# Performance work log

Hardware: AMD Instinct MI355X
Metric: run time of the kernel (lower is better)

## Reference

```python
import jax, jax.numpy as jnp
import numpy as np

N, E, C, K = 50000, 800000, 64, 8
D = C * K  # 512
NEG_SLOPE = 0.01  # torch leaky_relu default


def setup_inputs() -> dict:
    key = jax.random.key(0)
    ks = jax.random.split(key, 6)
    x = jax.random.normal(ks[0], (N, D), dtype=jnp.float32)
    edge_index = jax.random.randint(ks[1], (2, E), 0, N, dtype=jnp.int64)
    conv_W = jax.random.normal(ks[2], (K, C, C), dtype=jnp.float32) * (1.0 / np.sqrt(C))
    conv_b = jax.random.normal(ks[3], (K, C), dtype=jnp.float32) * 0.01
    W1 = jax.random.normal(ks[4], (D, D), dtype=jnp.float32) * (1.0 / np.sqrt(D))
    W2 = jax.random.normal(ks[5], (D, D), dtype=jnp.float32) * (1.0 / np.sqrt(D))
    return {"x": x, "edge_index": edge_index, "conv_W": conv_W,
            "conv_b": conv_b, "W1": W1, "W2": W2}


def _gcn_conv(xk, Wk, bk, src, dst, dinv, n):
    # PyG GCNConv: transform, then symmetric-normalized aggregation with self-loops,
    # then add bias.
    xt = xk @ Wk.T  # [N, C]
    norm = dinv[src] * dinv[dst]  # [E]
    agg = jax.ops.segment_sum(norm[:, None] * xt[src], dst, num_segments=n)
    agg = agg + (dinv * dinv)[:, None] * xt  # self-loop contribution
    return agg + bk


def reference(x, edge_index, conv_W, conv_b, W1, W2):
    n = x.shape[0]
    src, dst = edge_index[0], edge_index[1]
    # degree with self-loops (edge weight 1)
    deg = jax.ops.segment_sum(jnp.ones((E,), x.dtype), dst, num_segments=n) + 1.0
    dinv = deg ** -0.5
    xr = x.reshape(n, C, K)
    zs = [jax.nn.leaky_relu(_gcn_conv(xr[:, :, i], conv_W[i], conv_b[i], src, dst, dinv, n),
                            negative_slope=NEG_SLOPE)
          for i in range(K)]
    z = jnp.concatenate(zs, axis=1)  # [N, D]
    z = jax.nn.leaky_relu(z, negative_slope=NEG_SLOPE)
    # dropout is identity in eval mode (dr=12 is invalid for torch Dropout anyway)
    z_fc1 = z @ W1.T
    z_fc2 = z @ W2.T
    s = jnp.sum(z_fc1.T @ z_fc2, axis=0)  # [D]
    # softmax over axis 0 of a [1, D] tensor (as in the original code)
    gate = jax.nn.softmax((s / jnp.sqrt(jnp.asarray(D, x.dtype)))[None, :], axis=0)
    return z * gate
```

## Files before the change

### kernel.cpp

```cpp
#include <hip/hip_runtime.h>

#define NN 50000
#define EE 800000
#define KK 8
#define DD 512
#define CAP 64

typedef __attribute__((ext_vector_type(8))) short short8;
typedef __attribute__((ext_vector_type(4))) float f32x4;

__device__ __forceinline__ float leaky2(float v) {
    v = (v < 0.0f) ? 0.01f * v : v;
    v = (v < 0.0f) ? 0.01f * v : v;
    return v;
}

__device__ __forceinline__ unsigned short f2bf(float f) {
    unsigned u = __float_as_uint(f);
    u += 0x7fffu + ((u >> 16) & 1u);
    return (unsigned short)(u >> 16);
}
__device__ __forceinline__ float bf_lo(unsigned u) { return __uint_as_float(u << 16); }
__device__ __forceinline__ float bf_hi(unsigned u) { return __uint_as_float(u & 0xffff0000u); }

__global__ void k_zero(int* __restrict__ cnt, int* __restrict__ cursor) {
    int i = blockIdx.x * 256 + threadIdx.x;
    if (i < NN) { cnt[i] = 0; cursor[i] = 0; }
}

__global__ void k_count(const int* __restrict__ ei, int* __restrict__ cnt) {
    int e = blockIdx.x * 256 + threadIdx.x;
    if (e < EE) atomicAdd(&cnt[ei[EE + e]], 1);
}

__global__ void k_dinv(const int* __restrict__ cnt, float* __restrict__ dinv) {
    int i = blockIdx.x * 256 + threadIdx.x;
    if (i < NN) dinv[i] = rsqrtf((float)cnt[i] + 1.0f);
}

__global__ void k_wconv(const float* __restrict__ W, unsigned short* __restrict__ Wbf) {
    int i = blockIdx.x * 256 + threadIdx.x;
    if (i < KK * 64 * 64) Wbf[i] = f2bf(W[i]);
}

__global__ void k_fill(const int* __restrict__ ei, const float* __restrict__ dinv,
                       int* __restrict__ cursor, uint2* __restrict__ bw) {
    int e = blockIdx.x * 256 + threadIdx.x;
    if (e < EE) {
        int s = ei[e];
        int d = ei[EE + e];
        int p = atomicAdd(&cursor[d], 1);
        if (p < CAP) {
            uint2 v; v.x = (unsigned)s; v.y = __float_as_uint(dinv[s] * dinv[d]);
            bw[(size_t)d * CAP + p] = v;
        }
    }
}

__global__ __launch_bounds__(256) void k_transform(const float* __restrict__ x,
                                                   const unsigned short* __restrict__ Wbf,
                                                   unsigned short* __restrict__ xt) {
    __shared__ unsigned short lxT[32 * 8 * 64];
    const int t = threadIdx.x;
    const int n0 = blockIdx.x * 32;

    const float4* x4 = (const float4*)x;
    #pragma unroll
    for (int i = 0; i < 16; i++) {
        int idx = i * 256 + t;
        int n = idx >> 7;
        int q = idx & 127;
        int n_eff = n0 + n; if (n_eff >= NN) n_eff = NN - 1;
        float4 v = x4[(size_t)n_eff * 128 + q];
        int c = q >> 1;
        int k0 = (q & 1) * 4;
        unsigned short* p = &lxT[(n * 8 + k0) * 64 + c];
        p[0] = f2bf(v.x); p[64] = f2bf(v.y); p[128] = f2bf(v.z); p[192] = f2bf(v.w);
    }
    __syncthreads();

    const int wv   = t >> 6;
    const int lane = t & 63;
    const int l15  = lane & 15;
    const int quad = lane >> 4;
    const f32x4 zero = {0.f, 0.f, 0.f, 0.f};

    #pragma unroll
    for (int kk = 0; kk < 2; kk++) {
        const int k = wv * 2 + kk;
        short8 afr[4][2];
        #pragma unroll
        for (int jt = 0; jt < 4; jt++)
            #pragma unroll
            for (int ks = 0; ks < 2; ks++)
                afr[jt][ks] = *(const short8*)&Wbf[k * 4096 + (jt * 16 + l15) * 64 + ks * 32 + quad * 8];

        #pragma unroll
        for (int ng = 0; ng < 2; ng++) {
            short8 bfr[2];
            #pragma unroll
            for (int ks = 0; ks < 2; ks++)
                bfr[ks] = *(const short8*)&lxT[((ng * 16 + l15) * 8 + k) * 64 + ks * 32 + quad * 8];
            f32x4 acc[4];
            #pragma unroll
            for (int jt = 0; jt < 4; jt++) {
                acc[jt] = zero;
                acc[jt] = __builtin_amdgcn_mfma_f32_16x16x32_bf16(afr[jt][0], bfr[0], acc[jt], 0, 0, 0);
                acc[jt] = __builtin_amdgcn_mfma_f32_16x16x32_bf16(afr[jt][1], bfr[1], acc[jt], 0, 0, 0);
            }
            const int node = n0 + ng * 16 + l15;
            if (node < NN) {
                #pragma unroll
                for (int jt = 0; jt < 4; jt++) {
                    ushort4 h;
                    h.x = f2bf(acc[jt][0]); h.y = f2bf(acc[jt][1]);
                    h.z = f2bf(acc[jt][2]); h.w = f2bf(acc[jt][3]);
                    *(ushort4*)&xt[(size_t)node * DD + k * 64 + jt * 16 + quad * 4] = h;
                }
            }
        }
    }
}

__global__ __launch_bounds__(256) void k_agg(const unsigned short* __restrict__ xt,
                                             const float* __restrict__ dinv,
                                             const int* __restrict__ cnt,
                                             const uint2* __restrict__ bw,
                                             const float* __restrict__ bias,
                                             float* __restrict__ out) {
    const int n = blockIdx.x * 4 + (threadIdx.x >> 6);
    const int lane = threadIdx.x & 63;
    const float dn = dinv[n];
    int cn = cnt[n]; if (cn > CAP) cn = CAP;

    const uint4* xt4 = (const uint4*)xt;
    uint4 a = xt4[(size_t)n * 64 + lane];
    const float s0 = dn * dn;
    float acc[8];
    acc[0] = bf_lo(a.x) * s0; acc[1] = bf_hi(a.x) * s0;
    acc[2] = bf_lo(a.y) * s0; acc[3] = bf_hi(a.y) * s0;
    acc[4] = bf_lo(a.z) * s0; acc[5] = bf_hi(a.z) * s0;
    acc[6] = bf_lo(a.w) * s0; acc[7] = bf_hi(a.w) * s0;

    const uint2* bk = bw + (size_t)n * CAP;
    for (int i = 0; i < cn; i++) {
        uint2 e = bk[i];
        int s = (int)e.x;
        float w = __uint_as_float(e.y);
        uint4 v = xt4[(size_t)s * 64 + lane];
        acc[0] += w * bf_lo(v.x); acc[1] += w * bf_hi(v.x);
        acc[2] += w * bf_lo(v.y); acc[3] += w * bf_hi(v.y);
        acc[4] += w * bf_lo(v.z); acc[5] += w * bf_hi(v.z);
        acc[6] += w * bf_lo(v.w); acc[7] += w * bf_hi(v.w);
    }

    const float4* b4 = (const float4*)bias;
    float4 b0 = b4[lane * 2], b1 = b4[lane * 2 + 1];
    float4 r0, r1;
    r0.x = leaky2(acc[0] + b0.x); r0.y = leaky2(acc[1] + b0.y);
    r0.z = leaky2(acc[2] + b0.z); r0.w = leaky2(acc[3] + b0.w);
    r1.x = leaky2(acc[4] + b1.x); r1.y = leaky2(acc[5] + b1.y);
    r1.z = leaky2(acc[6] + b1.z); r1.w = leaky2(acc[7] + b1.w);
    float4* o4 = (float4*)(out + (size_t)n * DD);
    o4[lane * 2] = r0;
    o4[lane * 2 + 1] = r1;
}

extern "C" void kernel_launch(void* const* d_in, const int* in_sizes, int n_in,
                              void* d_out, int out_size, void* d_ws, size_t ws_size,
                              hipStream_t stream) {
    const float* x  = (const float*)d_in[0];
    const int*   ei = (const int*)d_in[1];
    const float* W  = (const float*)d_in[2];
    const float* b  = (const float*)d_in[3];
    float* out = (float*)d_out;

    unsigned short* xt = (unsigned short*)d_ws;
    float* dinv   = (float*)(xt + (size_t)NN * DD);
    int*   cnt    = (int*)(dinv + NN);
    int*   cursor = cnt + NN;
    uint2* bw     = (uint2*)(cursor + NN);
    unsigned short* wbf = (unsigned short*)(bw + (size_t)NN * CAP);

    k_zero <<<(NN + 255) / 256, 256, 0, stream>>>(cnt, cursor);
    k_count<<<(EE + 255) / 256, 256, 0, stream>>>(ei, cnt);
    k_wconv<<<(KK * 64 * 64 + 255) / 256, 256, 0, stream>>>(W, wbf);
    k_dinv <<<(NN + 255) / 256, 256, 0, stream>>>(cnt, dinv);
    k_fill <<<(EE + 255) / 256, 256, 0, stream>>>(ei, dinv, cursor, bw);
    k_transform<<<(NN + 31) / 32, 256, 0, stream>>>(x, wbf, xt);
    k_agg<<<NN / 4, 256, 0, stream>>>(xt, dinv, cnt, bw, b, out);
}
```

Baseline: 425.1 us.

## Derive degree from fill cursor, store only source indices, prefetch agg gathers

```diff
diff --git a/kernel.cpp b/kernel.cpp
--- a/kernel.cpp
+++ b/kernel.cpp
@@ -23,19 +23,16 @@
 __device__ __forceinline__ float bf_lo(unsigned u) { return __uint_as_float(u << 16); }
 __device__ __forceinline__ float bf_hi(unsigned u) { return __uint_as_float(u & 0xffff0000u); }
 
-__global__ void k_zero(int* __restrict__ cnt, int* __restrict__ cursor) {
+__device__ __forceinline__ void fma8(float acc[8], float w, uint4 v) {
+    acc[0] += w * bf_lo(v.x); acc[1] += w * bf_hi(v.x);
+    acc[2] += w * bf_lo(v.y); acc[3] += w * bf_hi(v.y);
+    acc[4] += w * bf_lo(v.z); acc[5] += w * bf_hi(v.z);
+    acc[6] += w * bf_lo(v.w); acc[7] += w * bf_hi(v.w);
+}
+
+__global__ void k_zero(int* __restrict__ cursor) {
     int i = blockIdx.x * 256 + threadIdx.x;
-    if (i < NN) { cnt[i] = 0; cursor[i] = 0; }
-}
-
-__global__ void k_count(const int* __restrict__ ei, int* __restrict__ cnt) {
-    int e = blockIdx.x * 256 + threadIdx.x;
-    if (e < EE) atomicAdd(&cnt[ei[EE + e]], 1);
-}
-
-__global__ void k_dinv(const int* __restrict__ cnt, float* __restrict__ dinv) {
-    int i = blockIdx.x * 256 + threadIdx.x;
-    if (i < NN) dinv[i] = rsqrtf((float)cnt[i] + 1.0f);
+    if (i < NN) cursor[i] = 0;
 }
 
 __global__ void k_wconv(const float* __restrict__ W, unsigned short* __restrict__ Wbf) {
@@ -43,18 +40,20 @@
     if (i < KK * 64 * 64) Wbf[i] = f2bf(W[i]);
 }
 
-__global__ void k_fill(const int* __restrict__ ei, const float* __restrict__ dinv,
-                       int* __restrict__ cursor, uint2* __restrict__ bw) {
+__global__ void k_fill(const int* __restrict__ ei, int* __restrict__ cursor,
+                       int* __restrict__ bw) {
     int e = blockIdx.x * 256 + threadIdx.x;
     if (e < EE) {
         int s = ei[e];
         int d = ei[EE + e];
         int p = atomicAdd(&cursor[d], 1);
-        if (p < CAP) {
-            uint2 v; v.x = (unsigned)s; v.y = __float_as_uint(dinv[s] * dinv[d]);
-            bw[(size_t)d * CAP + p] = v;
-        }
-    }
+        if (p < CAP) bw[(size_t)d * CAP + p] = s;
+    }
+}
+
+__global__ void k_dinv(const int* __restrict__ cursor, float* __restrict__ dinv) {
+    int i = blockIdx.x * 256 + threadIdx.x;
+    if (i < NN) dinv[i] = rsqrtf((float)cursor[i] + 1.0f);
 }
 
 __global__ __launch_bounds__(256) void k_transform(const float* __restrict__ x,
@@ -124,46 +123,58 @@
 
 __global__ __launch_bounds__(256) void k_agg(const unsigned short* __restrict__ xt,
                                              const float* __restrict__ dinv,
-                                             const int* __restrict__ cnt,
-                                             const uint2* __restrict__ bw,
+                                             const int* __restrict__ cursor,
+                                             const int* __restrict__ bw,
                                              const float* __restrict__ bias,
                                              float* __restrict__ out) {
-    const int n = blockIdx.x * 4 + (threadIdx.x >> 6);
+    const int n = __builtin_amdgcn_readfirstlane(blockIdx.x * 4 + (threadIdx.x >> 6));
     const int lane = threadIdx.x & 63;
     const float dn = dinv[n];
-    int cn = cnt[n]; if (cn > CAP) cn = CAP;
+    int cn = cursor[n]; if (cn > CAP) cn = CAP;
 
     const uint4* xt4 = (const uint4*)xt;
     uint4 a = xt4[(size_t)n * 64 + lane];
-    const float s0 = dn * dn;
+    const float sw = dn * dn;
     float acc[8];
-    acc[0] = bf_lo(a.x) * s0; acc[1] = bf_hi(a.x) * s0;
-    acc[2] = bf_lo(a.y) * s0; acc[3] = bf_hi(a.y) * s0;
-    acc[4] = bf_lo(a.z) * s0; acc[5] = bf_hi(a.z) * s0;
-    acc[6] = bf_lo(a.w) * s0; acc[7] = bf_hi(a.w) * s0;
-
-    const uint2* bk = bw + (size_t)n * CAP;
-    for (int i = 0; i < cn; i++) {
-        uint2 e = bk[i];
-        int s = (int)e.x;
-        float w = __uint_as_float(e.y);
+    acc[0] = bf_lo(a.x) * sw; acc[1] = bf_hi(a.x) * sw;
+    acc[2] = bf_lo(a.y) * sw; acc[3] = bf_hi(a.y) * sw;
+    acc[4] = bf_lo(a.z) * sw; acc[5] = bf_hi(a.z) * sw;
+    acc[6] = bf_lo(a.w) * sw; acc[7] = bf_hi(a.w) * sw;
+
+    const int* bk = bw + (size_t)n * CAP;
+    int i = 0;
+    if (cn >= 2) {
+        int sa = bk[0], sb = bk[1];
+        uint4 va = xt4[(size_t)sa * 64 + lane];
+        uint4 vb = xt4[(size_t)sb * 64 + lane];
+        float wa = dn * dinv[sa], wb = dn * dinv[sb];
+        for (i = 2; i + 1 < cn; i += 2) {
+            int sc = bk[i], sd = bk[i + 1];
+            uint4 vc = xt4[(size_t)sc * 64 + lane];
+            uint4 vd = xt4[(size_t)sd * 64 + lane];
+            float wc = dn * dinv[sc], wd = dn * dinv[sd];
+            fma8(acc, wa, va); fma8(acc, wb, vb);
+            wa = wc; wb = wd; va = vc; vb = vd;
+        }
+        fma8(acc, wa, va); fma8(acc, wb, vb);
+    }
+    for (; i < cn; ++i) {
+        int s = bk[i];
         uint4 v = xt4[(size_t)s * 64 + lane];
-        acc[0] += w * bf_lo(v.x); acc[1] += w * bf_hi(v.x);
-        acc[2] += w * bf_lo(v.y); acc[3] += w * bf_hi(v.y);
-        acc[4] += w * bf_lo(v.z); acc[5] += w * bf_hi(v.z);
-        acc[6] += w * bf_lo(v.w); acc[7] += w * bf_hi(v.w);
+        float w = dn * dinv[s];
+        fma8(acc, w, v);
     }
 
     const float4* b4 = (const float4*)bias;
     float4 b0 = b4[lane * 2], b1 = b4[lane * 2 + 1];
-    float4 r0, r1;
-    r0.x = leaky2(acc[0] + b0.x); r0.y = leaky2(acc[1] + b0.y);
-    r0.z = leaky2(acc[2] + b0.z); r0.w = leaky2(acc[3] + b0.w);
-    r1.x = leaky2(acc[4] + b1.x); r1.y = leaky2(acc[5] + b1.y);
-    r1.z = leaky2(acc[6] + b1.z); r1.w = leaky2(acc[7] + b1.w);
-    float4* o4 = (float4*)(out + (size_t)n * DD);
-    o4[lane * 2] = r0;
-    o4[lane * 2 + 1] = r1;
+    f32x4 r0, r1;
+    r0[0] = leaky2(acc[0] + b0.x); r0[1] = leaky2(acc[1] + b0.y);
+    r0[2] = leaky2(acc[2] + b0.z); r0[3] = leaky2(acc[3] + b0.w);
+    r1[0] = leaky2(acc[4] + b1.x); r1[1] = leaky2(acc[5] + b1.y);
+    r1[2] = leaky2(acc[6] + b1.z); r1[3] = leaky2(acc[7] + b1.w);
+    f32x4* o4 = (f32x4*)(out + (size_t)n * DD);
+    __builtin_nontemporal_store(r0, o4 + lane * 2);
+    __builtin_nontemporal_store(r1, o4 + lane * 2 + 1);
 }
 
 extern "C" void kernel_launch(void* const* d_in, const int* in_sizes, int n_in,
@@ -177,16 +188,14 @@
 
     unsigned short* xt = (unsigned short*)d_ws;
     float* dinv   = (float*)(xt + (size_t)NN * DD);
-    int*   cnt    = (int*)(dinv + NN);
-    int*   cursor = cnt + NN;
-    uint2* bw     = (uint2*)(cursor + NN);
+    int*   cursor = (int*)(dinv + NN);
+    int*   bw     = cursor + NN;
     unsigned short* wbf = (unsigned short*)(bw + (size_t)NN * CAP);
 
-    k_zero <<<(NN + 255) / 256, 256, 0, stream>>>(cnt, cursor);
-    k_count<<<(EE + 255) / 256, 256, 0, stream>>>(ei, cnt);
+    k_zero <<<(NN + 255) / 256, 256, 0, stream>>>(cursor);
     k_wconv<<<(KK * 64 * 64 + 255) / 256, 256, 0, stream>>>(W, wbf);
-    k_dinv <<<(NN + 255) / 256, 256, 0, stream>>>(cnt, dinv);
-    k_fill <<<(EE + 255) / 256, 256, 0, stream>>>(ei, dinv, cursor, bw);
+    k_fill <<<(EE + 255) / 256, 256, 0, stream>>>(ei, cursor, bw);
+    k_dinv <<<(NN + 255) / 256, 256, 0, stream>>>(cursor, dinv);
     k_transform<<<(NN + 31) / 32, 256, 0, stream>>>(x, wbf, xt);
-    k_agg<<<NN / 4, 256, 0, stream>>>(xt, dinv, cnt, bw, b, out);
-}
+    k_agg<<<NN / 4, 256, 0, stream>>>(xt, dinv, cursor, bw, b, out);
+}
```

New measurement: 382.0 us. 1.11x faster.
